# Optimization experiments

Measured on AMD Instinct MI355X. Metric: run time of the kernel, lower is better.

Reference implementation:

```python
import jax, jax.numpy as jnp
import numpy as np

B, D, C, H = 4096, 64, 16, 512   # batch, state dim, conditional dim, MLP hidden
NBIJ, NSTEPS = 2, 8              # stacked FFJORD bijectors, fixed RK4 steps over t in [0,1]


def setup_inputs() -> dict:
    key = jax.random.key(0)
    ks = jax.random.split(key, 8)
    g = lambda k, shape, scale: (jax.random.normal(k, shape, jnp.float32) * scale).astype(jnp.float32)
    return {
        "x": jax.random.normal(ks[0], (B, D), jnp.float32),
        "cond": jax.random.normal(ks[1], (B, C), jnp.float32),
        "eps": jax.random.normal(ks[2], (NBIJ, B, D), jnp.float32),  # Hutchinson probes, one per bijector
        "W1": g(ks[3], (NBIJ, D + C + 1, H), (D + C + 1) ** -0.5),
        "b1": jnp.zeros((NBIJ, H), jnp.float32),
        "W2": g(ks[4], (NBIJ, H, H), H ** -0.5),
        "b2": jnp.zeros((NBIJ, H), jnp.float32),
        "W3": g(ks[5], (NBIJ, H, D), H ** -0.5),
        "b3": jnp.zeros((NBIJ, D), jnp.float32),
    }


def _mlp(t, y, cond, W1, b1, W2, b2, W3, b3):
    # state_time_derivative_fn(t, x, conditional_input=cond) -> [B, D]
    tcol = jnp.full((y.shape[0], 1), t, y.dtype)
    h = jnp.tanh(jnp.concatenate([y, cond, tcol], axis=-1) @ W1 + b1)
    h = jnp.tanh(h @ W2 + b2)
    return h @ W3 + b3


def _integrate(x, cond, eps, params):
    # Augmented ODE: dy/dt = f(t,y), d(logdet)/dt = tr(df/dy) ~= eps^T J eps (Hutchinson)
    dt = jnp.float32(1.0 / NSTEPS)

    def aug(t, y):
        f = lambda z: _mlp(t, z, cond, *params)
        out, vjp_fn = jax.vjp(f, y)
        (epsJ,) = vjp_fn(eps)
        return out, jnp.sum(epsJ * eps, axis=-1)

    def step(carry, i):
        y, ld = carry
        t = i * dt
        k1, l1 = aug(t, y)
        k2, l2 = aug(t + 0.5 * dt, y + (0.5 * dt) * k1)
        k3, l3 = aug(t + 0.5 * dt, y + (0.5 * dt) * k2)
        k4, l4 = aug(t + dt, y + dt * k3)
        y = y + (dt / 6.0) * (k1 + 2.0 * k2 + 2.0 * k3 + k4)
        ld = ld + (dt / 6.0) * (l1 + 2.0 * l2 + 2.0 * l3 + l4)
        return (y, ld), None

    ld0 = jnp.zeros((x.shape[0],), x.dtype)
    (y, ld), _ = jax.lax.scan(step, (x, ld0), jnp.arange(NSTEPS, dtype=x.dtype))
    return y, ld


def reference(x, cond, eps, W1, b1, W2, b2, W3, b3):
    # Chain forward: bijector0 then bijector1 (tfb.Chain(reversed(...)) applies in build order)
    y = x
    ld = jnp.zeros((x.shape[0],), x.dtype)
    for ib in range(NBIJ):
        params = (W1[ib], b1[ib], W2[ib], b2[ib], W3[ib], b3[ib])
        y, d = _integrate(y, cond, eps[ib], params)
        ld = ld + d
    # augmented output: transformed state + accumulated log|det J|
    return jnp.concatenate([y, ld[:, None]], axis=-1)
```

## Files before the change

kernel.cpp:

```cpp
#include <hip/hip_runtime.h>


typedef __attribute__((ext_vector_type(8))) short short8;
typedef __attribute__((ext_vector_type(4))) float f32x4;
typedef __attribute__((ext_vector_type(4))) int int4v;

#define MFMA_B16(a, b, c) __builtin_amdgcn_mfma_f32_16x16x32_bf16((a), (b), (c), 0, 0, 0)
#define MFMA_I8(a, b, c)  __builtin_amdgcn_mfma_i32_16x16x64_i8((a), (b), (c), 0, 0, 0)

__device__ __forceinline__ unsigned short f2bf(float f) {
  union { float f; unsigned u; } v; v.f = f;
  return (unsigned short)((v.u + 0x7FFFu + ((v.u >> 16) & 1u)) >> 16);
}
__device__ __forceinline__ float bf2f(unsigned short u) {
  union { unsigned u; float f; } v; v.u = ((unsigned)u) << 16; return v.f;
}
__device__ __forceinline__ float fast_tanh(float x) {
  float e = __expf(2.f * x);
  return 1.f - 2.f * __builtin_amdgcn_rcpf(e + 1.f);
}


__global__ void prep_scales(const float* __restrict__ W2, float* __restrict__ sc) {
  int idx = blockIdx.x * 256 + threadIdx.x;
  if (idx >= 1024) return;
  int ib = idx >> 9, n = idx & 511;
  const float* W = W2 + (size_t)ib * 262144;
  float m = 0.f;
  for (int k = 0; k < 512; ++k) m = fmaxf(m, fabsf(W[(size_t)k * 512 + n]));
  sc[idx] = fmaxf(m, 1e-8f);
}

__global__ void prep_bf16(const float* __restrict__ W1, const float* __restrict__ W2,
                          const float* __restrict__ W3, unsigned short* __restrict__ ws) {
  int o = blockIdx.x * 256 + threadIdx.x;
  char* ws8 = (char*)ws;
  const float* sc = (const float*)(ws8 + 1114112);
  if (o < 98304) {
    int ib = o / 49152, r = o % 49152, n = r / 96, k = r % 96;
    ws[o] = (k < 81) ? f2bf(W1[(size_t)ib * 41472 + k * 512 + n]) : (unsigned short)0;
  } else if (o < 622592) {
    int b = o - 98304;
    int ib = b / 262144, b2 = b % 262144;
    int p = b2 / 32768, r2 = b2 % 32768, n = r2 / 64, kk = r2 & 63;
    int k = p * 64 + (kk ^ (((n >> 1) & 3) << 4));
    float w = W2[(size_t)ib * 262144 + (size_t)k * 512 + n];
    float s = sc[ib * 512 + n];
    int q = (int)rintf(w * (127.f / s));
    q = q > 127 ? 127 : (q < -127 ? -127 : q);
    ws8[196608 + b] = (char)q;
  } else if (o < 688128) {
    int o2 = o - 622592;
    int ib = o2 / 32768, r = o2 % 32768, n = r / 512, k = r % 512;
    ws[360448 + o2] = f2bf(W3[(size_t)ib * 32768 + k * 64 + n]);
  } else if (o < 753664) {
    int o2 = o - 688128;
    ws[425984 + o2] = f2bf(W3[o2]);
  } else if (o < 819200) {
    int o2 = o - 753664;
    int ib = o2 / 32768, r = o2 % 32768, h = r / 64, d = r % 64;
    ws[491520 + o2] = f2bf(W1[(size_t)ib * 41472 + d * 512 + h]);
  }
}

#define ZS 104
#define HS 520
#define H8 528
#define INV2 (1.f / 16129.f)

#define ISSUE_STAGE(WP, KS, BUF) do {                                                   \
    const char* _s = (WP) + (KS) * 32768 + (wave << 11) + (lane << 4);                  \
    char* _d = &Bst[(BUF)][wave << 11];                                                 \
    __builtin_amdgcn_global_load_lds(                                                   \
        (const __attribute__((address_space(1))) void*)_s,                              \
        (__attribute__((address_space(3))) void*)_d, 16, 0, 0);                         \
    __builtin_amdgcn_global_load_lds(                                                   \
        (const __attribute__((address_space(1))) void*)(_s + 1024),                     \
        (__attribute__((address_space(3))) void*)(_d + 1024), 16, 0, 0);                \
  } while (0)

__global__ __launch_bounds__(1024) void ffjord_mfma(
    const float* __restrict__ x, const float* __restrict__ cond, const float* __restrict__ eps,
    const float* __restrict__ b1g, const float* __restrict__ b2g, const float* __restrict__ b3g,
    const unsigned short* __restrict__ ws, float* __restrict__ out) {
  __shared__ unsigned short zA[16 * ZS];
  __shared__ __align__(16) char h1A8[16 * H8];
  __shared__ __align__(16) char vA8[16 * H8];
  __shared__ unsigned short h2A[16 * HS];
  __shared__ __align__(16) char Bst[3][32768];
  __shared__ float f_s[16][64];
  __shared__ float l_row[16], ld_row[16], ldacc[16];
  __shared__ int sgu[16];

  const int t = threadIdx.x;
  const int wave = t >> 6;
  const int lane = t & 63;
  const int lane15 = lane & 15;
  const int q8 = (lane >> 4) * 8;
  const int q16 = (lane >> 4) * 16;
  const int rowb = q8 >> 1;
  const int row0 = blockIdx.x * 16;
  const int ws32 = wave * 32;
  const int nt3 = wave & 3;
  const int kb3 = (wave >> 2) * 128;
  const int tm = t >> 6, td = t & 63;

  const int kk2b = q16 ^ (((lane15 >> 1) & 3) << 4);

  float ycur, ytmp, yacc = 0.f;
  {
    float xv = x[(size_t)(row0 + tm) * 64 + td];
    ycur = xv; ytmp = xv;
  }
  if (t < 512) {
    int m = t >> 5, kk = t & 31;
    zA[m * ZS + 64 + kk] = (kk < 16) ? f2bf(cond[(size_t)(row0 + m) * 16 + kk]) : (unsigned short)0;
  }
  if (t < 16) { ld_row[t] = 0.f; l_row[t] = 0.f; }

  const float dt = 0.125f;
  const float w06 = dt / 6.f, w13 = dt / 3.f;
  const char* wsb = (const char*)ws;

  for (int ib = 0; ib < 2; ++ib) {
    const unsigned short* W1f = ws + ib * 49152;
    const char* W2f8 = wsb + 196608 + ib * 262144;
    const unsigned short* W3f = ws + 360448 + ib * 32768;
    const unsigned short* W3b = ws + 425984 + ib * 32768;
    const unsigned short* W1u = ws + 491520 + ib * 32768;
    const float* scf = (const float*)(wsb + 1114112) + ib * 512;
    const float* b1b = b1g + ib * 512;
    const float* b2b = b2g + ib * 512;
    const float* b3b = b3g + ib * 64;

    zA[tm * ZS + td] = f2bf(eps[((size_t)ib * 4096 + row0 + tm) * 64 + td]);
    if (t < 16) sgu[t] = 0;
    __syncthreads();

    float e3r[8], ur[8];
    {
      f32x4 a0 = {0,0,0,0}, a1 = {0,0,0,0};
      f32x4 u0 = {0,0,0,0}, u1 = {0,0,0,0};
      const unsigned short* ap = zA + lane15 * ZS + q8;
      const unsigned short* wp3 = W3b + (size_t)(ws32 + lane15) * 64 + q8;
      const unsigned short* wpu = W1u + (size_t)(ws32 + lane15) * 64 + q8;
      #pragma unroll
      for (int kk = 0; kk < 64; kk += 32) {
        short8 a = *(const short8*)(ap + kk);
        a0 = MFMA_B16(a, *(const short8*)(wp3 + kk),           a0);
        a1 = MFMA_B16(a, *(const short8*)(wp3 + 16 * 64 + kk), a1);
        u0 = MFMA_B16(a, *(const short8*)(wpu + kk),           u0);
        u1 = MFMA_B16(a, *(const short8*)(wpu + 16 * 64 + kk), u1);
      }
      #pragma unroll
      for (int rg = 0; rg < 4; ++rg) {
        e3r[rg] = a0[rg]; e3r[4 + rg] = a1[rg];
        ur[rg] = u0[rg];  ur[4 + rg] = u1[rg];
      }
      #pragma unroll
      for (int rg = 0; rg < 4; ++rg) {
        float mr = fmaxf(fabsf(ur[rg]), fabsf(ur[4 + rg]));
        #pragma unroll
        for (int o = 1; o < 16; o <<= 1) mr = fmaxf(mr, __shfl_xor(mr, o));
        if (lane15 == 0) atomicMax(&sgu[rowb + rg], __float_as_int(mr));
      }
    }
    __syncthreads();

    float su_[4], qsv[4];
    #pragma unroll
    for (int rg = 0; rg < 4; ++rg) {
      float sg = fmaxf(__int_as_float(sgu[rowb + rg]), 1e-20f);
      su_[rg] = sg * INV2;
      qsv[rg] = 127.f / sg;
    }

    for (int it = 0; it < 32; ++it) {
      const int s = it & 3;
      const float te = (it >> 2) * dt + ((s == 0) ? 0.f : (s == 3) ? dt : 0.5f * dt);

      if (it > 0) {
        int sp = (it - 1) & 3;
        float fv = f_s[tm][td] + b3b[td];
        if (sp == 0)      { yacc = ycur + w06 * fv; ytmp = ycur + 0.5f * dt * fv; }
        else if (sp == 1) { yacc += w13 * fv;       ytmp = ycur + 0.5f * dt * fv; }
        else if (sp == 2) { yacc += w13 * fv;       ytmp = ycur + dt * fv; }
        else              { float yn = yacc + w06 * fv; ycur = yn; ytmp = yn; }
      }
      zA[tm * ZS + td] = f2bf(ytmp);
      f_s[tm][td] = 0.f;
      if (t < 16) {
        if (it > 0) {
          int sp = (it - 1) & 3;
          float lv = l_row[t];
          if (sp == 0)      ldacc[t] = w06 * lv;
          else if (sp < 3)  ldacc[t] += w13 * lv;
          else              ld_row[t] += ldacc[t] + w06 * lv;
        }
        l_row[t] = 0.f;
        zA[t * ZS + 80] = f2bf(te);
      }
      if (it == 0) { ISSUE_STAGE(W2f8, 0, 0); ISSUE_STAGE(W2f8, 1, 1); ISSUE_STAGE(W2f8, 2, 2); }
      __syncthreads();

      {
        f32x4 a0 = {0,0,0,0}, a1 = {0,0,0,0};
        const unsigned short* ap = zA + lane15 * ZS + q8;
        const unsigned short* wp = W1f + (size_t)(ws32 + lane15) * 96 + q8;
        #pragma unroll
        for (int k0 = 0; k0 < 96; k0 += 32) {
          short8 a = *(const short8*)(ap + k0);
          a0 = MFMA_B16(a, *(const short8*)(wp + k0),           a0);
          a1 = MFMA_B16(a, *(const short8*)(wp + 16 * 96 + k0), a1);
        }
        #pragma unroll
        for (int tl = 0; tl < 2; ++tl) {
          int n = ws32 + tl * 16 + lane15;
          float bias = b1b[n];
          f32x4 ac = tl ? a1 : a0;
          #pragma unroll
          for (int rg = 0; rg < 4; ++rg) {
            float th = fast_tanh(ac[rg] + bias);
            int off = (rowb + rg) * H8 + n;
            h1A8[off] = (char)__float2int_rn(th * 127.f);
            float v = (1.f - th * th) * ur[tl * 4 + rg];
            vA8[off] = (char)__float2int_rn(v * qsv[rg]);
          }
        }
      }
      __syncthreads();

      {
        int4v ha0 = {0,0,0,0}, ha1 = {0,0,0,0}, wa0 = {0,0,0,0}, wa1 = {0,0,0,0};
        const char* aph = h1A8 + lane15 * H8;
        const char* apv = vA8 + lane15 * H8;
        #pragma unroll
        for (int ks = 0; ks < 8; ++ks) {
          if (ks < 6)       asm volatile("s_waitcnt vmcnt(4)" ::: "memory");
          else if (ks == 6) asm volatile("s_waitcnt vmcnt(2)" ::: "memory");
          else              asm volatile("s_waitcnt vmcnt(0)" ::: "memory");
          const char* bq = &Bst[ks % 3][wave << 11];
          int4v ah = *(const int4v*)(aph + ks * 64 + q16);
          int4v av = *(const int4v*)(apv + ks * 64 + q16);
          int4v b0 = *(const int4v*)(bq + lane15 * 64 + kk2b);
          int4v b1 = *(const int4v*)(bq + (16 + lane15) * 64 + kk2b);
          asm volatile("s_waitcnt lgkmcnt(0)" ::: "memory");
          __builtin_amdgcn_sched_barrier(0);
          if (ks + 3 < 8) { ISSUE_STAGE(W2f8, ks + 3, (ks + 3) % 3); }
          ha0 = MFMA_I8(ah, b0, ha0);
          ha1 = MFMA_I8(ah, b1, ha1);
          wa0 = MFMA_I8(av, b0, wa0);
          wa1 = MFMA_I8(av, b1, wa1);
        }
        float p0 = 0.f, p1 = 0.f, p2 = 0.f, p3 = 0.f;
        #pragma unroll
        for (int tl = 0; tl < 2; ++tl) {
          int n = ws32 + tl * 16 + lane15;
          float bias = b2b[n];
          float dq = scf[n] * INV2;
          float dqw = scf[n];
          int4v hac = tl ? ha1 : ha0;
          int4v wac = tl ? wa1 : wa0;
          #pragma unroll
          for (int rg = 0; rg < 4; ++rg) {
            float h = fast_tanh((float)hac[rg] * dq + bias);
            h2A[(rowb + rg) * HS + n] = f2bf(h);
            float g2 = e3r[tl * 4 + rg] * (1.f - h * h);
            float w = (float)wac[rg] * dqw * su_[rg];
            float pc = g2 * w;
            if (rg == 0) p0 += pc; else if (rg == 1) p1 += pc;
            else if (rg == 2) p2 += pc; else p3 += pc;
          }
        }
        #pragma unroll
        for (int o = 1; o < 16; o <<= 1) {
          p0 += __shfl_xor(p0, o); p1 += __shfl_xor(p1, o);
          p2 += __shfl_xor(p2, o); p3 += __shfl_xor(p3, o);
        }
        if (lane15 == 0) {
          atomicAdd(&l_row[rowb + 0], p0); atomicAdd(&l_row[rowb + 1], p1);
          atomicAdd(&l_row[rowb + 2], p2); atomicAdd(&l_row[rowb + 3], p3);
        }
      }
      __syncthreads();

      if (it < 31) { ISSUE_STAGE(W2f8, 0, 0); ISSUE_STAGE(W2f8, 1, 1); ISSUE_STAGE(W2f8, 2, 2); }
      {
        f32x4 c0 = {0,0,0,0};
        const unsigned short* ap3 = h2A + lane15 * HS + kb3 + q8;
        const unsigned short* wp3 = W3f + (size_t)(nt3 * 16 + lane15) * 512 + kb3 + q8;
        #pragma unroll
        for (int kk = 0; kk < 128; kk += 32)
          c0 = MFMA_B16(*(const short8*)(ap3 + kk), *(const short8*)(wp3 + kk), c0);
        #pragma unroll
        for (int rg = 0; rg < 4; ++rg)
          atomicAdd(&f_s[rowb + rg][nt3 * 16 + lane15], c0[rg]);
      }
      __syncthreads();
    }

    {
      float fv = f_s[tm][td] + b3b[td];
      float yn = yacc + w06 * fv;
      ycur = yn; ytmp = yn;
    }
    if (t < 16) { ld_row[t] += ldacc[t] + w06 * l_row[t]; l_row[t] = 0.f; }
    __syncthreads();
  }

  out[(size_t)(row0 + tm) * 65 + td] = ycur;
  if (t < 16) out[(size_t)(row0 + t) * 65 + 64] = ld_row[t];
}

extern "C" void kernel_launch(void* const* d_in, const int* in_sizes, int n_in,
                              void* d_out, int out_size, void* d_ws, size_t ws_size,
                              hipStream_t stream) {
  (void)in_sizes; (void)n_in; (void)out_size; (void)ws_size;
  const float* x    = (const float*)d_in[0];
  const float* cond = (const float*)d_in[1];
  const float* eps  = (const float*)d_in[2];
  const float* W1   = (const float*)d_in[3];
  const float* b1   = (const float*)d_in[4];
  const float* W2   = (const float*)d_in[5];
  const float* b2   = (const float*)d_in[6];
  const float* W3   = (const float*)d_in[7];
  const float* b3   = (const float*)d_in[8];
  float* out = (float*)d_out;
  unsigned short* ws = (unsigned short*)d_ws;

  prep_scales<<<4, 256, 0, stream>>>(W2, (float*)((char*)ws + 1114112));
  const int prep_total = 819200;
  prep_bf16<<<(prep_total + 255) / 256, 256, 0, stream>>>(W1, W2, W3, ws);
  ffjord_mfma<<<256, 1024, 0, stream>>>(x, cond, eps, b1, b2, b3, ws, out);
}
```

Before: 1.065 ms.

## Quantize layer-1 and layer-3 matmuls to int8 and precompute conditional bias

The first-layer y-part and the third-layer matmul move from bf16 MFMA to int8 MFMA. They use per-row dynamic scales for the state and per-column weight scales. The constant conditional-input contribution plus b1 is computed once per bijector into an LDS bias table, and the time column becomes a scalar fma term, which removes per-step K padding. This cuts MFMA count and LDS traffic per RK stage, at the cost of more quantization error in the state path and a larger LDS footprint.

Result: slower. 1.167 ms (+9.6%).

```diff
diff --git a/kernel.cpp b/kernel.cpp
--- a/kernel.cpp
+++ b/kernel.cpp
@@ -21,50 +21,79 @@
 }
 
 
-__global__ void prep_scales(const float* __restrict__ W2, float* __restrict__ sc) {
+__global__ void prep_scales(const float* __restrict__ W1, const float* __restrict__ W2,
+                            const float* __restrict__ W3, float* __restrict__ wsf) {
   int idx = blockIdx.x * 256 + threadIdx.x;
-  if (idx >= 1024) return;
-  int ib = idx >> 9, n = idx & 511;
-  const float* W = W2 + (size_t)ib * 262144;
-  float m = 0.f;
-  for (int k = 0; k < 512; ++k) m = fmaxf(m, fabsf(W[(size_t)k * 512 + n]));
-  sc[idx] = fmaxf(m, 1e-8f);
-}
-
-__global__ void prep_bf16(const float* __restrict__ W1, const float* __restrict__ W2,
+  if (idx < 1024) {
+    int ib = idx >> 9, n = idx & 511;
+    const float* W = W2 + (size_t)ib * 262144;
+    float m = 0.f;
+    for (int k = 0; k < 512; ++k) m = fmaxf(m, fabsf(W[(size_t)k * 512 + n]));
+    wsf[246784 + idx] = fmaxf(m, 1e-8f);
+  } else if (idx < 2048) {
+    int i2 = idx - 1024, ib = i2 >> 9, n = i2 & 511;
+    const float* W = W1 + (size_t)ib * 41472;
+    float m = 0.f;
+    for (int k = 0; k < 64; ++k) m = fmaxf(m, fabsf(W[(size_t)k * 512 + n]));
+    wsf[247808 + i2] = fmaxf(m, 1e-8f);
+  } else if (idx < 2176) {
+    int i2 = idx - 2048, ib = i2 >> 6, d = i2 & 63;
+    const float* W = W3 + (size_t)ib * 32768;
+    float m = 0.f;
+    for (int h = 0; h < 512; ++h) m = fmaxf(m, fabsf(W[(size_t)h * 64 + d]));
+    wsf[248832 + i2] = fmaxf(m, 1e-8f);
+  }
+}
+
+__global__ void prep_pack(const float* __restrict__ W1, const float* __restrict__ W2,
                           const float* __restrict__ W3, unsigned short* __restrict__ ws) {
   int o = blockIdx.x * 256 + threadIdx.x;
   char* ws8 = (char*)ws;
-  const float* sc = (const float*)(ws8 + 1114112);
-  if (o < 98304) {
-    int ib = o / 49152, r = o % 49152, n = r / 96, k = r % 96;
-    ws[o] = (k < 81) ? f2bf(W1[(size_t)ib * 41472 + k * 512 + n]) : (unsigned short)0;
-  } else if (o < 622592) {
-    int b = o - 98304;
-    int ib = b / 262144, b2 = b % 262144;
-    int p = b2 / 32768, r2 = b2 % 32768, n = r2 / 64, kk = r2 & 63;
+  const float* wsf = (const float*)ws;
+  if (o < 524288) {
+    int ib = o >> 18, b2 = o & 262143;
+    int p = b2 >> 15, r2 = b2 & 32767, n = r2 >> 6, kk = r2 & 63;
     int k = p * 64 + (kk ^ (((n >> 1) & 3) << 4));
     float w = W2[(size_t)ib * 262144 + (size_t)k * 512 + n];
-    float s = sc[ib * 512 + n];
+    float s = wsf[246784 + ib * 512 + n];
     int q = (int)rintf(w * (127.f / s));
     q = q > 127 ? 127 : (q < -127 ? -127 : q);
-    ws8[196608 + b] = (char)q;
-  } else if (o < 688128) {
-    int o2 = o - 622592;
-    int ib = o2 / 32768, r = o2 % 32768, n = r / 512, k = r % 512;
-    ws[360448 + o2] = f2bf(W3[(size_t)ib * 32768 + k * 64 + n]);
-  } else if (o < 753664) {
-    int o2 = o - 688128;
-    ws[425984 + o2] = f2bf(W3[o2]);
+    ws8[o] = (char)q;
+  } else if (o < 589824) {
+    int o2 = o - 524288;
+    int ib = o2 >> 15, r = o2 & 32767, n = r >> 6, k = r & 63;
+    float w = W1[(size_t)ib * 41472 + (size_t)k * 512 + n];
+    float s = wsf[247808 + ib * 512 + n];
+    int q = (int)rintf(w * (127.f / s));
+    q = q > 127 ? 127 : (q < -127 ? -127 : q);
+    ws8[524288 + o2] = (char)q;
+  } else if (o < 655360) {
+    int o2 = o - 589824;
+    int ib = o2 >> 15, r = o2 & 32767, d = r >> 9, h = r & 511;
+    float w = W3[(size_t)ib * 32768 + (size_t)h * 64 + d];
+    float s = wsf[248832 + ib * 64 + d];
+    int q = (int)rintf(w * (127.f / s));
+    q = q > 127 ? 127 : (q < -127 ? -127 : q);
+    ws8[589824 + o2] = (char)q;
+  } else if (o < 720896) {
+    int o2 = o - 655360;
+    ws[327680 + o2] = f2bf(W3[o2]);
+  } else if (o < 786432) {
+    int o2 = o - 720896;
+    int ib = o2 >> 15, r = o2 & 32767, h = r >> 6, d = r & 63;
+    ws[393216 + o2] = f2bf(W1[(size_t)ib * 41472 + (size_t)d * 512 + h]);
   } else if (o < 819200) {
-    int o2 = o - 753664;
-    int ib = o2 / 32768, r = o2 % 32768, h = r / 64, d = r % 64;
-    ws[491520 + o2] = f2bf(W1[(size_t)ib * 41472 + d * 512 + h]);
+    int o2 = o - 786432;
+    int ib = o2 >> 14, r = o2 & 16383, n = r >> 5, c = r & 31;
+    ws[458752 + o2] = (c < 16) ? f2bf(W1[(size_t)ib * 41472 + (size_t)(64 + c) * 512 + n])
+                               : (unsigned short)0;
+  } else if (o < 820224) {
+    int o2 = o - 819200;
+    int ib = o2 >> 9, n = o2 & 511;
+    ((float*)ws)[245760 + o2] = W1[(size_t)ib * 41472 + 80 * 512 + n];
   }
 }
 
-#define ZS 104
-#define HS 520
 #define H8 528
 #define INV2 (1.f / 16129.f)
 
@@ -83,14 +112,15 @@
     const float* __restrict__ x, const float* __restrict__ cond, const float* __restrict__ eps,
     const float* __restrict__ b1g, const float* __restrict__ b2g, const float* __restrict__ b3g,
     const unsigned short* __restrict__ ws, float* __restrict__ out) {
-  __shared__ unsigned short zA[16 * ZS];
-  __shared__ __align__(16) char h1A8[16 * H8];
-  __shared__ __align__(16) char vA8[16 * H8];
-  __shared__ unsigned short h2A[16 * HS];
+  __shared__ __align__(16) char scratch[2 * 16 * H8];
+  __shared__ __align__(16) char h2A8[16 * H8];
+  __shared__ __align__(16) char zA8[16 * 64];
+  __shared__ float cbias[16][512];
   __shared__ __align__(16) char Bst[3][32768];
   __shared__ float f_s[16][64];
   __shared__ float l_row[16], ld_row[16], ldacc[16];
   __shared__ int sgu[16];
+  __shared__ float sy_s[16];
 
   const int t = threadIdx.x;
   const int wave = t >> 6;
@@ -107,41 +137,57 @@
 
   const int kk2b = q16 ^ (((lane15 >> 1) & 3) << 4);
 
+  char* h1A8 = scratch;
+  char* vA8  = scratch + 16 * H8;
+
   float ycur, ytmp, yacc = 0.f;
-  {
-    float xv = x[(size_t)(row0 + tm) * 64 + td];
-    ycur = xv; ytmp = xv;
-  }
-  if (t < 512) {
-    int m = t >> 5, kk = t & 31;
-    zA[m * ZS + 64 + kk] = (kk < 16) ? f2bf(cond[(size_t)(row0 + m) * 16 + kk]) : (unsigned short)0;
-  }
+  { float xv = x[(size_t)(row0 + tm) * 64 + td]; ycur = xv; ytmp = xv; }
   if (t < 16) { ld_row[t] = 0.f; l_row[t] = 0.f; }
 
   const float dt = 0.125f;
   const float w06 = dt / 6.f, w13 = dt / 3.f;
   const char* wsb = (const char*)ws;
+  const float* wsf = (const float*)ws;
 
   for (int ib = 0; ib < 2; ++ib) {
-    const unsigned short* W1f = ws + ib * 49152;
-    const char* W2f8 = wsb + 196608 + ib * 262144;
-    const unsigned short* W3f = ws + 360448 + ib * 32768;
-    const unsigned short* W3b = ws + 425984 + ib * 32768;
-    const unsigned short* W1u = ws + 491520 + ib * 32768;
-    const float* scf = (const float*)(wsb + 1114112) + ib * 512;
+    const char* W2f8 = wsb + ib * 262144;
+    const char* W1y8 = wsb + 524288 + ib * 32768;
+    const char* W3f8 = wsb + 589824 + ib * 32768;
+    const unsigned short* W3b = ws + 327680 + ib * 32768;
+    const unsigned short* W1u = ws + 393216 + ib * 32768;
+    const unsigned short* W1c = ws + 458752 + ib * 16384;
+    const float* w1tg = wsf + 245760 + ib * 512;
+    const float* s2g  = wsf + 246784 + ib * 512;
+    const float* s1g  = wsf + 247808 + ib * 512;
+    const float* s3g  = wsf + 248832 + ib * 64;
     const float* b1b = b1g + ib * 512;
     const float* b2b = b2g + ib * 512;
     const float* b3b = b3g + ib * 64;
 
-    zA[tm * ZS + td] = f2bf(eps[((size_t)ib * 4096 + row0 + tm) * 64 + td]);
+    const int n0 = ws32 + lane15, n1 = n0 + 16;
+    const float t1_0 = s1g[n0] * INV2, t1_1 = s1g[n1] * INV2;
+    const float w1t0 = w1tg[n0],       w1t1 = w1tg[n1];
+    const float b2_0 = b2b[n0],        b2_1 = b2b[n1];
+    const float s2_0 = s2g[n0],        s2_1 = s2g[n1];
+    const float dq2_0 = s2_0 * INV2,   dq2_1 = s2_1 * INV2;
+    const float dq3  = s3g[nt3 * 16 + lane15] * INV2;
+    const float fb3  = b3b[td];
+
+    unsigned short* epsA  = (unsigned short*)scratch;
+    unsigned short* condA = (unsigned short*)(scratch + 4096);
+    epsA[tm * 72 + td] = f2bf(eps[((size_t)ib * 4096 + row0 + tm) * 64 + td]);
+    if (t < 512) {
+      int m = t >> 5, kk = t & 31;
+      condA[m * 32 + kk] = (kk < 16) ? f2bf(cond[(size_t)(row0 + m) * 16 + kk])
+                                     : (unsigned short)0;
+    }
     if (t < 16) sgu[t] = 0;
     __syncthreads();
 
     float e3r[8], ur[8];
     {
-      f32x4 a0 = {0,0,0,0}, a1 = {0,0,0,0};
-      f32x4 u0 = {0,0,0,0}, u1 = {0,0,0,0};
-      const unsigned short* ap = zA + lane15 * ZS + q8;
+      f32x4 a0 = {0,0,0,0}, a1 = {0,0,0,0}, u0 = {0,0,0,0}, u1 = {0,0,0,0};
+      const unsigned short* ap  = epsA + lane15 * 72 + q8;
       const unsigned short* wp3 = W3b + (size_t)(ws32 + lane15) * 64 + q8;
       const unsigned short* wpu = W1u + (size_t)(ws32 + lane15) * 64 + q8;
       #pragma unroll
@@ -164,6 +210,20 @@
         for (int o = 1; o < 16; o <<= 1) mr = fmaxf(mr, __shfl_xor(mr, o));
         if (lane15 == 0) atomicMax(&sgu[rowb + rg], __float_as_int(mr));
       }
+      f32x4 c0 = {0,0,0,0}, c1 = {0,0,0,0};
+      short8 ac = *(const short8*)(condA + lane15 * 32 + q8);
+      const unsigned short* wpc = W1c + (size_t)(ws32 + lane15) * 32 + q8;
+      c0 = MFMA_B16(ac, *(const short8*)wpc,             c0);
+      c1 = MFMA_B16(ac, *(const short8*)(wpc + 16 * 32), c1);
+      #pragma unroll
+      for (int tl = 0; tl < 2; ++tl) {
+        int n = tl ? n1 : n0;
+        float bb = b1b[n];
+        f32x4 cc = tl ? c1 : c0;
+        #pragma unroll
+        for (int rg = 0; rg < 4; ++rg)
+          cbias[rowb + rg][n] = cc[rg] + bb;
+      }
     }
     __syncthreads();
 
@@ -181,14 +241,21 @@
 
       if (it > 0) {
         int sp = (it - 1) & 3;
-        float fv = f_s[tm][td] + b3b[td];
+        float fv = f_s[tm][td] + fb3;
         if (sp == 0)      { yacc = ycur + w06 * fv; ytmp = ycur + 0.5f * dt * fv; }
         else if (sp == 1) { yacc += w13 * fv;       ytmp = ycur + 0.5f * dt * fv; }
         else if (sp == 2) { yacc += w13 * fv;       ytmp = ycur + dt * fv; }
         else              { float yn = yacc + w06 * fv; ycur = yn; ytmp = yn; }
       }
-      zA[tm * ZS + td] = f2bf(ytmp);
       f_s[tm][td] = 0.f;
+      {
+        float my = fabsf(ytmp);
+        #pragma unroll
+        for (int o = 1; o < 64; o <<= 1) my = fmaxf(my, __shfl_xor(my, o));
+        my = fmaxf(my, 1e-20f);
+        if (lane == 0) sy_s[tm] = my;
+        zA8[tm * 64 + td] = (char)__float2int_rn(ytmp * (127.f / my));
+      }
       if (t < 16) {
         if (it > 0) {
           int sp = (it - 1) & 3;
@@ -198,30 +265,29 @@
           else              ld_row[t] += ldacc[t] + w06 * lv;
         }
         l_row[t] = 0.f;
-        zA[t * ZS + 80] = f2bf(te);
       }
       if (it == 0) { ISSUE_STAGE(W2f8, 0, 0); ISSUE_STAGE(W2f8, 1, 1); ISSUE_STAGE(W2f8, 2, 2); }
       __syncthreads();
 
       {
-        f32x4 a0 = {0,0,0,0}, a1 = {0,0,0,0};
-        const unsigned short* ap = zA + lane15 * ZS + q8;
-        const unsigned short* wp = W1f + (size_t)(ws32 + lane15) * 96 + q8;
-        #pragma unroll
-        for (int k0 = 0; k0 < 96; k0 += 32) {
-          short8 a = *(const short8*)(ap + k0);
-          a0 = MFMA_B16(a, *(const short8*)(wp + k0),           a0);
-          a1 = MFMA_B16(a, *(const short8*)(wp + 16 * 96 + k0), a1);
-        }
+        int4v a = *(const int4v*)(zA8 + lane15 * 64 + q16);
+        int4v b0v = *(const int4v*)(W1y8 + (size_t)n0 * 64 + q16);
+        int4v b1v = *(const int4v*)(W1y8 + (size_t)n1 * 64 + q16);
+        int4v z4 = {0, 0, 0, 0};
+        int4v ac0 = MFMA_I8(a, b0v, z4);
+        int4v ac1 = MFMA_I8(a, b1v, z4);
         #pragma unroll
         for (int tl = 0; tl < 2; ++tl) {
-          int n = ws32 + tl * 16 + lane15;
-          float bias = b1b[n];
-          f32x4 ac = tl ? a1 : a0;
+          int n = tl ? n1 : n0;
+          float t1 = tl ? t1_1 : t1_0;
+          float wt = tl ? w1t1 : w1t0;
+          int4v ac = tl ? ac1 : ac0;
           #pragma unroll
           for (int rg = 0; rg < 4; ++rg) {
-            float th = fast_tanh(ac[rg] + bias);
-            int off = (rowb + rg) * H8 + n;
+            int m = rowb + rg;
+            float pre = (float)ac[rg] * (sy_s[m] * t1) + cbias[m][n] + te * wt;
+            float th = fast_tanh(pre);
+            int off = m * H8 + n;
             h1A8[off] = (char)__float2int_rn(th * 127.f);
             float v = (1.f - th * th) * ur[tl * 4 + rg];
             vA8[off] = (char)__float2int_rn(v * qsv[rg]);
@@ -255,16 +321,16 @@
         float p0 = 0.f, p1 = 0.f, p2 = 0.f, p3 = 0.f;
         #pragma unroll
         for (int tl = 0; tl < 2; ++tl) {
-          int n = ws32 + tl * 16 + lane15;
-          float bias = b2b[n];
-          float dq = scf[n] * INV2;
-          float dqw = scf[n];
+          int n = tl ? n1 : n0;
+          float bias = tl ? b2_1 : b2_0;
+          float dq = tl ? dq2_1 : dq2_0;
+          float dqw = tl ? s2_1 : s2_0;
           int4v hac = tl ? ha1 : ha0;
           int4v wac = tl ? wa1 : wa0;
           #pragma unroll
           for (int rg = 0; rg < 4; ++rg) {
             float h = fast_tanh((float)hac[rg] * dq + bias);
-            h2A[(rowb + rg) * HS + n] = f2bf(h);
+            h2A8[(rowb + rg) * H8 + n] = (char)__float2int_rn(h * 127.f);
             float g2 = e3r[tl * 4 + rg] * (1.f - h * h);
             float w = (float)wac[rg] * dqw * su_[rg];
             float pc = g2 * w;
@@ -286,21 +352,20 @@
 
       if (it < 31) { ISSUE_STAGE(W2f8, 0, 0); ISSUE_STAGE(W2f8, 1, 1); ISSUE_STAGE(W2f8, 2, 2); }
       {
-        f32x4 c0 = {0,0,0,0};
-        const unsigned short* ap3 = h2A + lane15 * HS + kb3 + q8;
-        const unsigned short* wp3 = W3f + (size_t)(nt3 * 16 + lane15) * 512 + kb3 + q8;
-        #pragma unroll
-        for (int kk = 0; kk < 128; kk += 32)
-          c0 = MFMA_B16(*(const short8*)(ap3 + kk), *(const short8*)(wp3 + kk), c0);
+        const char* ap3 = h2A8 + lane15 * H8 + kb3;
+        const char* wp3 = W3f8 + (size_t)(nt3 * 16 + lane15) * 512 + kb3;
+        int4v z4 = {0, 0, 0, 0};
+        int4v c = MFMA_I8(*(const int4v*)(ap3 + q16), *(const int4v*)(wp3 + q16), z4);
+        c = MFMA_I8(*(const int4v*)(ap3 + 64 + q16), *(const int4v*)(wp3 + 64 + q16), c);
         #pragma unroll
         for (int rg = 0; rg < 4; ++rg)
-          atomicAdd(&f_s[rowb + rg][nt3 * 16 + lane15], c0[rg]);
+          atomicAdd(&f_s[rowb + rg][nt3 * 16 + lane15], (float)c[rg] * dq3);
       }
       __syncthreads();
     }
 
     {
-      float fv = f_s[tm][td] + b3b[td];
+      float fv = f_s[tm][td] + fb3;
       float yn = yacc + w06 * fv;
       ycur = yn; ytmp = yn;
     }
@@ -328,8 +393,8 @@
   float* out = (float*)d_out;
   unsigned short* ws = (unsigned short*)d_ws;
 
-  prep_scales<<<4, 256, 0, stream>>>(W2, (float*)((char*)ws + 1114112));
-  const int prep_total = 819200;
-  prep_bf16<<<(prep_total + 255) / 256, 256, 0, stream>>>(W1, W2, W3, ws);
+  prep_scales<<<9, 256, 0, stream>>>(W1, W2, W3, (float*)ws);
+  const int prep_total = 820224;
+  prep_pack<<<(prep_total + 255) / 256, 256, 0, stream>>>(W1, W2, W3, ws);
   ffjord_mfma<<<256, 1024, 0, stream>>>(x, cond, eps, b1, b2, b3, ws, out);
 }
```
